# Optimization experiments

Hardware: AMD Instinct MI355X
Metric: run time of the kernel (lower is better)

## Reference

```python
import jax, jax.numpy as jnp
import numpy as np

B, L, D, H = 4, 1024, 1024, 16
HD = D // H
SCALE = 1.0 / np.sqrt(HD)
NOISE_PROB = 0.05
NOISE_SCALE = 0.1


def _linear(x, w, b):
    # torch nn.Linear convention: y = x @ W^T + b, W: [out, in]
    return x @ w.T + b


def _quantum_noise(key, real, imag, p=NOISE_PROB, s=NOISE_SCALE):
    """Phase flips, amplitude noise, and measurement dropout on a complex
    tensor represented as (real, imag). Deterministic given `key`."""
    k_phase, k_amp, k_nr, k_ni, k_meas = jax.random.split(key, 5)
    shape = real.shape
    flip = jnp.where(jax.random.uniform(k_phase, shape) < p, -1.0, 1.0)
    amp_mask = (jax.random.uniform(k_amp, shape) < p).astype(real.dtype)
    new_r = real * flip + jax.random.normal(k_nr, shape, real.dtype) * s * amp_mask
    new_i = imag * flip + jax.random.normal(k_ni, shape, imag.dtype) * s * amp_mask
    keep = 1.0 - (jax.random.uniform(k_meas, shape) < p * 0.5).astype(real.dtype)
    return new_r * keep, new_i * keep


def _heads(t):
    # [B, L, D] -> [B, H, L, HD]
    b, l, _ = t.shape
    return t.reshape(b, l, H, HD).transpose(0, 2, 1, 3)


def setup_inputs() -> dict:
    key = jax.random.key(0)
    ks = jax.random.split(key, 16)
    inp = {
        "x_real": jax.random.normal(ks[0], (B, L, D), jnp.float32),
        "x_imag": jax.random.normal(ks[1], (B, L, D), jnp.float32),
        "mask": jnp.ones((B, L), jnp.int32),
    }
    names = ["qr", "qi", "kr", "ki", "vr", "vi", "or", "oi"]
    for i, n in enumerate(names):
        inp[n + "_w"] = jax.random.normal(ks[2 + i], (D, D), jnp.float32) * 0.02
        inp[n + "_b"] = jnp.zeros((D,), jnp.float32)
    ent = jnp.eye(H) + (jax.random.normal(ks[10], (H, H)) * 0.1) * (
        jax.random.uniform(ks[11], (H, H)) < 0.2
    ).astype(jnp.float32)
    inp["ent"] = ent
    return inp


def reference(x_real, x_imag, mask, qr_w, qr_b, qi_w, qi_b, kr_w, kr_b,
              ki_w, ki_b, vr_w, vr_b, vi_w, vi_b, or_w, or_b, oi_w, oi_b, ent):
    # complex Q/K/V: real part from x.real, imag part from x.imag
    q_r, q_i = _linear(x_real, qr_w, qr_b), _linear(x_imag, qi_w, qi_b)
    k_r, k_i = _linear(x_real, kr_w, kr_b), _linear(x_imag, ki_w, ki_b)
    v_r, v_i = _linear(x_real, vr_w, vr_b), _linear(x_imag, vi_w, vi_b)

    nkey = jax.random.key(1)
    q_r, q_i = _quantum_noise(jax.random.fold_in(nkey, 0), q_r, q_i)
    k_r, k_i = _quantum_noise(jax.random.fold_in(nkey, 1), k_r, k_i)
    v_r, v_i = _quantum_noise(jax.random.fold_in(nkey, 2), v_r, v_i)

    q_r, q_i, k_r, k_i, v_r, v_i = map(_heads, (q_r, q_i, k_r, k_i, v_r, v_i))

    # torch.einsum('bhld,hh->bhld') == per-head scaling by diag(ent)
    d = jnp.diagonal(ent)[None, :, None, None]
    q_r, q_i = q_r * d, q_i * d
    k_r, k_i = k_r * d, k_i * d

    # Re(q . conj(k)) interference score: [B, H, Lq, Lk]
    scores = (jnp.einsum("bhqd,bhkd->bhqk", q_r, k_r)
              + jnp.einsum("bhqd,bhkd->bhqk", q_i, k_i)) * SCALE
    scores = jnp.where(mask[:, None, None, :] == 0, -1e9, scores)
    attn = jax.nn.softmax(scores, axis=-1)

    out_r = jnp.einsum("bhqk,bhkd->bhqd", attn, v_r)
    out_i = jnp.einsum("bhqk,bhkd->bhqd", attn, v_i)
    out_r = out_r.transpose(0, 2, 1, 3).reshape(x_real.shape)
    out_i = out_i.transpose(0, 2, 1, 3).reshape(x_real.shape)

    out_real = _linear(out_r, or_w, or_b)
    out_imag = _linear(out_i, oi_w, oi_b)
    return out_real, out_imag, attn
```

## Files before the change

### kernel.cpp

```cpp
#include <hip/hip_runtime.h>
#include <cstdint>

#define PARTITIONABLE 1

static constexpr int Bsz = 4, Lsz = 1024, Dsz = 1024, Hn = 16, HDsz = 64;
static constexpr size_t ELEMS = (size_t)Bsz * Lsz * Dsz;
static constexpr uint32_t HALF_N = (uint32_t)(ELEMS / 2);
static constexpr float SCALE = 0.125f;
static constexpr float P_NOISE = 0.05f;
static constexpr float S_NOISE = 0.1f;
static constexpr size_t MBy = 1024 * 1024;

typedef unsigned short u16;
typedef uint64_t u64;
typedef __attribute__((ext_vector_type(8))) short short8v;
typedef __attribute__((ext_vector_type(4))) float floatx4;
typedef __attribute__((ext_vector_type(4))) unsigned int uint4v;

__device__ __forceinline__ void gload16(const u16* g, u16* l) {
  __builtin_amdgcn_global_load_lds(
      (const __attribute__((address_space(1))) void*)(g),
      (__attribute__((address_space(3))) void*)(l), 16, 0, 0);
}

__host__ __device__ __forceinline__ void tf2x32(uint32_t k0, uint32_t k1,
                                                uint32_t x0, uint32_t x1,
                                                uint32_t& o0, uint32_t& o1) {
  uint32_t ks2 = k0 ^ k1 ^ 0x1BD11BDAu;
  x0 += k0; x1 += k1;
#define TFR(r) { x0 += x1; x1 = (x1 << (r)) | (x1 >> (32 - (r))); x1 ^= x0; }
  TFR(13) TFR(15) TFR(26) TFR(6)
  x0 += k1; x1 += ks2 + 1u;
  TFR(17) TFR(29) TFR(16) TFR(24)
  x0 += ks2; x1 += k0 + 2u;
  TFR(13) TFR(15) TFR(26) TFR(6)
  x0 += k0; x1 += k1 + 3u;
  TFR(17) TFR(29) TFR(16) TFR(24)
  x0 += k1; x1 += ks2 + 4u;
  TFR(13) TFR(15) TFR(26) TFR(6)
  x0 += ks2; x1 += k0 + 5u;
#undef TFR
  o0 = x0; o1 = x1;
}

struct KeySet { uint32_t k[5][2]; };
struct AllKeys { KeySet t[3]; };

__device__ __forceinline__ uint32_t draw_bits(uint32_t k0, uint32_t k1, uint32_t idx) {
#if PARTITIONABLE
  uint32_t o0, o1; tf2x32(k0, k1, 0u, idx, o0, o1);
  return o0 ^ o1;
#else
  uint32_t o0, o1;
  if (idx < HALF_N) { tf2x32(k0, k1, idx, idx + HALF_N, o0, o1); return o0; }
  tf2x32(k0, k1, idx - HALF_N, idx, o0, o1); return o1;
#endif
}

__device__ __forceinline__ float unif01(uint32_t bits) {
  return __uint_as_float((bits >> 9) | 0x3f800000u) - 1.0f;
}

__device__ __forceinline__ float normal_from_bits(uint32_t bits) {
  const float LO = -0.99999994f;
  float f = unif01(bits);
  float x = fmaxf(LO, f * 2.0f + LO);
  float w = -log1pf(-x * x);
  float p;
  if (w < 5.0f) {
    w = w - 2.5f;
    p = 2.81022636e-08f;
    p = fmaf(p, w, 3.43273939e-07f);
    p = fmaf(p, w, -3.5233877e-06f);
    p = fmaf(p, w, -4.39150654e-06f);
    p = fmaf(p, w, 0.00021858087f);
    p = fmaf(p, w, -0.00125372503f);
    p = fmaf(p, w, -0.00417768164f);
    p = fmaf(p, w, 0.246640727f);
    p = fmaf(p, w, 1.50140941f);
  } else {
    w = sqrtf(w) - 3.0f;
    p = -0.000200214257f;
    p = fmaf(p, w, 0.000100950558f);
    p = fmaf(p, w, 0.00134934322f);
    p = fmaf(p, w, -0.00367342844f);
    p = fmaf(p, w, 0.00573950773f);
    p = fmaf(p, w, -0.0076224613f);
    p = fmaf(p, w, 0.00943887047f);
    p = fmaf(p, w, 1.00167406f);
    p = fmaf(p, w, 2.83297682f);
  }
  return 1.41421356f * (p * x);
}

__device__ __forceinline__ uint32_t bf16_rn(float f) {
  uint32_t u = __float_as_uint(f);
  return (u + 0x7FFFu + ((u >> 16) & 1u)) >> 16;
}
__device__ __forceinline__ float bf2f(uint32_t h) { return __uint_as_float(h << 16); }
__device__ __forceinline__ void cvt_split(float4 v, u64& hi, u64& lo) {
  uint32_t h0 = bf16_rn(v.x), h1 = bf16_rn(v.y), h2 = bf16_rn(v.z), h3 = bf16_rn(v.w);
  float r0 = v.x - bf2f(h0), r1 = v.y - bf2f(h1), r2 = v.z - bf2f(h2), r3 = v.w - bf2f(h3);
  uint32_t l0 = bf16_rn(r0), l1 = bf16_rn(r1), l2 = bf16_rn(r2), l3 = bf16_rn(r3);
  hi = (u64)h0 | ((u64)h1 << 16) | ((u64)h2 << 32) | ((u64)h3 << 48);
  lo = (u64)l0 | ((u64)l1 << 16) | ((u64)l2 << 32) | ((u64)l3 << 48);
}

__device__ __forceinline__ void mfma_tile(const u16* Ahs, const u16* Als,
                                          const u16* Bhs, const u16* Bls,
                                          int l, int wm, int wn, floatx4 acc[4][4]) {
#pragma unroll
  for (int c = 0; c < 2; ++c) {
    const int pr = (l ^ (l >> 4) ^ (c << 2)) & 63;
    short8v aH[4], aL[4], bH[4], bL[4];
#pragma unroll
    for (int t = 0; t < 4; ++t) {
      const int ia = ((c * 8 + wm * 4 + t) * 64 + pr) * 8;
      aH[t] = *(const short8v*)&Ahs[ia]; aL[t] = *(const short8v*)&Als[ia];
      const int ib = ((c * 8 + wn * 4 + t) * 64 + pr) * 8;
      bH[t] = *(const short8v*)&Bhs[ib]; bL[t] = *(const short8v*)&Bls[ib];
    }
#pragma unroll
    for (int mt = 0; mt < 4; ++mt)
#pragma unroll
      for (int nt = 0; nt < 4; ++nt) {
        acc[mt][nt] = __builtin_amdgcn_mfma_f32_16x16x32_bf16(aH[mt], bH[nt], acc[mt][nt], 0, 0, 0);
        acc[mt][nt] = __builtin_amdgcn_mfma_f32_16x16x32_bf16(aH[mt], bL[nt], acc[mt][nt], 0, 0, 0);
        acc[mt][nt] = __builtin_amdgcn_mfma_f32_16x16x32_bf16(aL[mt], bH[nt], acc[mt][nt], 0, 0, 0);
      }
  }
}

__global__ __launch_bounds__(256) void split_kernel(const float* __restrict__ src,
                                                    u16* __restrict__ dh,
                                                    u16* __restrict__ dl, int n4) {
  int i = blockIdx.x * 256 + (int)threadIdx.x;
  if (i >= n4) return;
  float4 v = ((const float4*)src)[i];
  u64 h, l; cvt_split(v, h, l);
  ((u64*)dh)[i] = h; ((u64*)dl)[i] = l;
}

struct GJob { const u16* Ah; const u16* Al; const u16* Wh; const u16* Wl;
              const float* Wf; const float* bias; float* Yf; u16* Yh; u16* Yl; };
struct GJobs { GJob j[6]; };

template<int MODE>
__global__ __launch_bounds__(256, 2) void gemm_kernel(GJobs jobs) {
  const GJob J = jobs.j[blockIdx.z];
  const int n0 = blockIdx.x * 128, m0 = blockIdx.y * 128;
  __shared__ u16 Ahs[8192], Als[8192], Bhs[8192], Bls[8192];
  const int tid = (int)threadIdx.x;
  const int q_st = tid >> 4, kq = tid & 15;
  const int c_st = kq >> 3, m2s = (kq >> 1) & 3, half = kq & 1;
  const int p_st = (q_st + 16 * m2s) ^ m2s ^ (c_st << 2);
  const int stBase = c_st * 4096 + p_st * 8 + half * 4;
  const int w = tid >> 6, l = tid & 63;
  const int cA = w >> 1, m2A = l >> 4;
  const int qA = (l ^ m2A ^ (cA << 2)) & 15;
  const int colA = cA * 32 + m2A * 8;
  const int tb = (w & 1) * 4;
  const int wm = w >> 1, wn = w & 1;

  floatx4 acc[4][4];
#pragma unroll
  for (int i = 0; i < 4; ++i)
#pragma unroll
    for (int j = 0; j < 4; ++j) acc[i][j] = (floatx4){0.f, 0.f, 0.f, 0.f};

  const u16* ahp = J.Ah + (size_t)(m0 + qA) * Dsz + colA;
  const u16* alp = J.Al + (size_t)(m0 + qA) * Dsz + colA;
  const u16* whp = (MODE == 0) ? J.Wh + (size_t)(n0 + qA) * Dsz + colA : nullptr;
  const u16* wlp = (MODE == 0) ? J.Wl + (size_t)(n0 + qA) * Dsz + colA : nullptr;
  const float* wrow = (MODE == 1) ? J.Wf + (size_t)(n0 + q_st) * Dsz + kq * 4 : nullptr;

  for (int k0 = 0; k0 < Dsz; k0 += 64) {
    __syncthreads();
#pragma unroll
    for (int i = 0; i < 4; ++i) {
      const size_t go = (size_t)((tb + i) * 16) * Dsz + k0;
      gload16(ahp + go, &Ahs[(w * 4 + i) * 512]);
      gload16(alp + go, &Als[(w * 4 + i) * 512]);
      if (MODE == 0) {
        gload16(whp + go, &Bhs[(w * 4 + i) * 512]);
        gload16(wlp + go, &Bls[(w * 4 + i) * 512]);
      }
    }
    if (MODE == 1) {
#pragma unroll
      for (int rr = 0; rr < 8; ++rr) {
        float4 wb = *(const float4*)(wrow + (size_t)rr * 16 * Dsz + k0);
        u64 bh, bl; cvt_split(wb, bh, bl);
        const int off = stBase + rr * 512;
        *(u64*)&Bhs[off] = bh; *(u64*)&Bls[off] = bl;
      }
    }
    __syncthreads();
    mfma_tile(Ahs, Als, Bhs, Bls, l, wm, wn, acc);
  }
  const int colLane = l & 15, rquad = l >> 4;
#pragma unroll
  for (int nt = 0; nt < 4; ++nt) {
    const int col = n0 + wn * 64 + nt * 16 + colLane;
    const float bv = J.bias[col];
#pragma unroll
    for (int mt = 0; mt < 4; ++mt) {
      const int r0 = m0 + wm * 64 + mt * 16 + rquad * 4;
#pragma unroll
      for (int j = 0; j < 4; ++j) {
        float v = acc[mt][nt][j] + bv;
        if (MODE == 1) {
          J.Yf[(size_t)(r0 + j) * Dsz + col] = v;
        } else {
          uint32_t hi = bf16_rn(v);
          uint32_t lo = bf16_rn(v - bf2f(hi));
          J.Yh[(size_t)(r0 + j) * Dsz + col] = (u16)hi;
          J.Yl[(size_t)(r0 + j) * Dsz + col] = (u16)lo;
        }
      }
    }
  }
}

__global__ __launch_bounds__(256) void noise_kernel(
    u16* __restrict__ qhr, u16* __restrict__ qlr, u16* __restrict__ qhi, u16* __restrict__ qli,
    u16* __restrict__ khr, u16* __restrict__ klr, u16* __restrict__ khi, u16* __restrict__ kli,
    u16* __restrict__ vhr, u16* __restrict__ vlr, u16* __restrict__ vhi, u16* __restrict__ vli,
    const float* __restrict__ ent, AllKeys keys) {
  const uint32_t e = blockIdx.x * 256u + threadIdx.x;
  const int j = (int)blockIdx.y;
  u16 *rh, *rl, *ih, *il;
  if (j == 0) { rh = qhr; rl = qlr; ih = qhi; il = qli; }
  else if (j == 1) { rh = khr; rl = klr; ih = khi; il = kli; }
  else { rh = vhr; rl = vlr; ih = vhi; il = vli; }
  const KeySet& ks = keys.t[j];
  const uint32_t b_phase = draw_bits(ks.k[0][0], ks.k[0][1], e);
  const uint32_t b_amp   = draw_bits(ks.k[1][0], ks.k[1][1], e);
  const uint32_t b_nr    = draw_bits(ks.k[2][0], ks.k[2][1], e);
  const uint32_t b_ni    = draw_bits(ks.k[3][0], ks.k[3][1], e);
  const uint32_t b_meas  = draw_bits(ks.k[4][0], ks.k[4][1], e);
  const float flip = (unif01(b_phase) < P_NOISE) ? -1.0f : 1.0f;
  const float amp  = (unif01(b_amp)  < P_NOISE) ? 1.0f : 0.0f;
  const float keep = (unif01(b_meas) < P_NOISE * 0.5f) ? 0.0f : 1.0f;
  const float nr = normal_from_bits(b_nr);
  const float ni = normal_from_bits(b_ni);
  float r  = bf2f(rh[e]) + bf2f(rl[e]);
  float iv = bf2f(ih[e]) + bf2f(il[e]);
  r  = (r  * flip + nr * S_NOISE * amp) * keep;
  iv = (iv * flip + ni * S_NOISE * amp) * keep;
  if (j != 2) {
    const int h = ((int)e & (Dsz - 1)) >> 6;
    const float d = ent[h * Hn + h];
    r *= d; iv *= d;
  }
  uint32_t hr = bf16_rn(r);  rh[e] = (u16)hr; rl[e] = (u16)bf16_rn(r - bf2f(hr));
  uint32_t hi2 = bf16_rn(iv); ih[e] = (u16)hi2; il[e] = (u16)bf16_rn(iv - bf2f(hi2));
}

__global__ __launch_bounds__(256, 2) void scores_kernel(
    const u16* __restrict__ qhr, const u16* __restrict__ qlr,
    const u16* __restrict__ qhi, const u16* __restrict__ qli,
    const u16* __restrict__ khr, const u16* __restrict__ klr,
    const u16* __restrict__ khi, const u16* __restrict__ kli,
    const int* __restrict__ mask, float* __restrict__ attn) {
  const int bh = (int)blockIdx.z;
  const int b = bh >> 4, h = bh & 15;
  const int n0 = blockIdx.x * 128, m0 = blockIdx.y * 128;
  __shared__ u16 Ahs[8192], Als[8192], Bhs[8192], Bls[8192];
  const int tid = (int)threadIdx.x;
  const int w = tid >> 6, l = tid & 63;
  const int cA = w >> 1, m2A = l >> 4;
  const int qA = (l ^ m2A ^ (cA << 2)) & 15;
  const int colA = cA * 32 + m2A * 8;
  const int tb = (w & 1) * 4;
  const int wm = w >> 1, wn = w & 1;

  floatx4 acc[4][4];
#pragma unroll
  for (int i = 0; i < 4; ++i)
#pragma unroll
    for (int j = 0; j < 4; ++j) acc[i][j] = (floatx4){0.f, 0.f, 0.f, 0.f};

  const size_t abase = ((size_t)(b * Lsz) + m0 + qA) * Dsz + h * HDsz + colA;
  const size_t bbase = ((size_t)(b * Lsz) + n0 + qA) * Dsz + h * HDsz + colA;

#pragma unroll
  for (int s = 0; s < 2; ++s) {
    const u16* Ah = s ? qhi : qhr; const u16* Al = s ? qli : qlr;
    const u16* Bh = s ? khi : khr; const u16* Bl = s ? kli : klr;
    __syncthreads();
#pragma unroll
    for (int i = 0; i < 4; ++i) {
      const size_t go = (size_t)((tb + i) * 16) * Dsz;
      gload16(Ah + abase + go, &Ahs[(w * 4 + i) * 512]);
      gload16(Al + abase + go, &Als[(w * 4 + i) * 512]);
      gload16(Bh + bbase + go, &Bhs[(w * 4 + i) * 512]);
      gload16(Bl + bbase + go, &Bls[(w * 4 + i) * 512]);
    }
    __syncthreads();
    mfma_tile(Ahs, Als, Bhs, Bls, l, wm, wn, acc);
  }
  const int colLane = l & 15, rquad = l >> 4;
#pragma unroll
  for (int nt = 0; nt < 4; ++nt) {
    const int col = n0 + wn * 64 + nt * 16 + colLane;
    const int mv = mask[b * Lsz + col];
#pragma unroll
    for (int mt = 0; mt < 4; ++mt) {
      const int r0 = m0 + wm * 64 + mt * 16 + rquad * 4;
#pragma unroll
      for (int j = 0; j < 4; ++j)
        attn[((size_t)bh * Lsz + r0 + j) * Lsz + col] =
            (mv == 0) ? -1e9f : acc[mt][nt][j] * SCALE;
    }
  }
}

__global__ __launch_bounds__(256) void vtrans_kernel(
    const u16* __restrict__ vhr, const u16* __restrict__ vlr,
    const u16* __restrict__ vhi, const u16* __restrict__ vli,
    u16* __restrict__ vth, u16* __restrict__ vtl) {
  const int bh = (int)blockIdx.y;
  const int b = bh >> 4, h = bh & 15;
  const int k0 = blockIdx.x * 64;
  __shared__ uint32_t T[128 * 65];
  const int t = (int)threadIdx.x;
  const int krow = t >> 4, d4 = (t & 15) * 4;

#pragma unroll
  for (int src = 0; src < 2; ++src) {
    const u16* VH = src ? vhi : vhr;
    const u16* VL = src ? vli : vlr;
    const int nb = src * 64;
#pragma unroll
    for (int p = 0; p < 4; ++p) {
      const int k = p * 16 + krow;
      const size_t off = ((size_t)(b * Lsz) + k0 + k) * Dsz + h * HDsz + d4;
      u64 hv = *(const u64*)(VH + off);
      u64 lv = *(const u64*)(VL + off);
#pragma unroll
      for (int e = 0; e < 4; ++e) {
        uint32_t hi = (uint32_t)((hv >> (16 * e)) & 0xFFFFu);
        uint32_t lo = (uint32_t)((lv >> (16 * e)) & 0xFFFFu);
        T[(nb + d4 + e) * 65 + k] = lo | (hi << 16);
      }
    }
  }
  __syncthreads();
  const int n = t >> 1, hf = t & 1;
  const size_t rowb = ((size_t)bh * 128 + n) * Lsz + k0 + hf * 32;
#pragma unroll
  for (int g = 0; g < 4; ++g) {
    uint32_t wv[8];
#pragma unroll
    for (int u = 0; u < 8; ++u) wv[u] = T[n * 65 + hf * 32 + g * 8 + u];
    uint4v hvv, lvv;
    hvv.x = (wv[0] >> 16) | (wv[1] & 0xFFFF0000u);
    hvv.y = (wv[2] >> 16) | (wv[3] & 0xFFFF0000u);
    hvv.z = (wv[4] >> 16) | (wv[5] & 0xFFFF0000u);
    hvv.w = (wv[6] >> 16) | (wv[7] & 0xFFFF0000u);
    lvv.x = (wv[0] & 0xFFFFu) | (wv[1] << 16);
    lvv.y = (wv[2] & 0xFFFFu) | (wv[3] << 16);
    lvv.z = (wv[4] & 0xFFFFu) | (wv[5] << 16);
    lvv.w = (wv[6] & 0xFFFFu) | (wv[7] << 16);
    *(uint4v*)&vth[rowb + g * 8] = hvv;
    *(uint4v*)&vtl[rowb + g * 8] = lvv;
  }
}

__global__ __launch_bounds__(256) void rowstat_kernel(const float* __restrict__ S,
                                                      float* __restrict__ rowm,
                                                      float* __restrict__ rowsum) {
  const int wv = (int)threadIdx.x >> 6, lane = (int)threadIdx.x & 63;
  const size_t row = (size_t)blockIdx.x * 4 + wv;
  const float* p = S + row * Lsz;
  float4 v[4];
#pragma unroll
  for (int i = 0; i < 4; ++i) v[i] = *(const float4*)(p + i * 256 + lane * 4);
  float m = -3.402823466e38f;
#pragma unroll
  for (int i = 0; i < 4; ++i)
    m = fmaxf(m, fmaxf(fmaxf(v[i].x, v[i].y), fmaxf(v[i].z, v[i].w)));
#pragma unroll
  for (int d = 1; d < 64; d <<= 1) m = fmaxf(m, __shfl_xor(m, d));
  float s = 0.f;
#pragma unroll
  for (int i = 0; i < 4; ++i)
    s += expf(v[i].x - m) + expf(v[i].y - m) + expf(v[i].z - m) + expf(v[i].w - m);
#pragma unroll
  for (int d = 1; d < 64; d <<= 1) s += __shfl_xor(s, d);
  if (lane == 0) { rowm[row] = m; rowsum[row] = s; }
}

__global__ __launch_bounds__(256, 2) void pv_kernel(
    float* __restrict__ attn, const u16* __restrict__ vth, const u16* __restrict__ vtl,
    const float* __restrict__ rowm, const float* __restrict__ rowsum,
    u16* __restrict__ ohr, u16* __restrict__ olr,
    u16* __restrict__ ohi, u16* __restrict__ oli) {
  const int bh = (int)blockIdx.y;
  const int b = bh >> 4, h = bh & 15;
  const int m0 = blockIdx.x * 128;
  __shared__ u16 Ahs[8192], Als[8192], Bhs[8192], Bls[8192];
  const int tid = (int)threadIdx.x;
  const int q_st = tid >> 4, kq = tid & 15;
  const int c_st = kq >> 3, m2s = (kq >> 1) & 3, half = kq & 1;
  const int p_st = (q_st + 16 * m2s) ^ m2s ^ (c_st << 2);
  const int stBase = c_st * 4096 + p_st * 8 + half * 4;
  const int w = tid >> 6, l = tid & 63;
  const int cA = w >> 1, m2A = l >> 4;
  const int qA = (l ^ m2A ^ (cA << 2)) & 15;
  const int colA = cA * 32 + m2A * 8;
  const int tb = (w & 1) * 4;
  const int wm = w >> 1, wn = w & 1;

  float rmv[8], inv[8];
#pragma unroll
  for (int rr = 0; rr < 8; ++rr) {
    const int row = bh * Lsz + m0 + q_st + rr * 16;
    rmv[rr] = rowm[row]; inv[rr] = 1.0f / rowsum[row];
  }

  floatx4 acc[4][4];
#pragma unroll
  for (int i = 0; i < 4; ++i)
#pragma unroll
    for (int j = 0; j < 4; ++j) acc[i][j] = (floatx4){0.f, 0.f, 0.f, 0.f};

  float* arow = attn + ((size_t)bh * Lsz + m0 + q_st) * Lsz + kq * 4;
  const u16* bhp = vth + ((size_t)bh * 128 + qA) * Lsz + colA;
  const u16* blp = vtl + ((size_t)bh * 128 + qA) * Lsz + colA;

  for (int k0 = 0; k0 < Lsz; k0 += 64) {
    __syncthreads();
#pragma unroll
    for (int i = 0; i < 4; ++i) {
      const size_t go = (size_t)((tb + i) * 16) * Lsz + k0;
      gload16(bhp + go, &Bhs[(w * 4 + i) * 512]);
      gload16(blp + go, &Bls[(w * 4 + i) * 512]);
    }
#pragma unroll
    for (int rr = 0; rr < 8; ++rr) {
      float4 s4 = *(const float4*)(arow + (size_t)rr * 16 * Lsz + k0);
      float4 p4;
      p4.x = expf(s4.x - rmv[rr]) * inv[rr];
      p4.y = expf(s4.y - rmv[rr]) * inv[rr];
      p4.z = expf(s4.z - rmv[rr]) * inv[rr];
      p4.w = expf(s4.w - rmv[rr]) * inv[rr];
      *(float4*)(arow + (size_t)rr * 16 * Lsz + k0) = p4;
      u64 ah, al; cvt_split(p4, ah, al);
      const int off = stBase + rr * 512;
      *(u64*)&Ahs[off] = ah; *(u64*)&Als[off] = al;
    }
    __syncthreads();
    mfma_tile(Ahs, Als, Bhs, Bls, l, wm, wn, acc);
  }
  const int colLane = l & 15, rquad = l >> 4;
#pragma unroll
  for (int nt = 0; nt < 4; ++nt) {
    const int col = wn * 64 + nt * 16 + colLane;
    u16* oh = (col < 64) ? ohr : ohi;
    u16* ol = (col < 64) ? olr : oli;
    const int dcol = col & 63;
#pragma unroll
    for (int mt = 0; mt < 4; ++mt) {
      const int r0 = m0 + wm * 64 + mt * 16 + rquad * 4;
#pragma unroll
      for (int j = 0; j < 4; ++j) {
        float v = acc[mt][nt][j];
        uint32_t hi = bf16_rn(v);
        uint32_t lo = bf16_rn(v - bf2f(hi));
        const size_t oidx = ((size_t)(b * Lsz) + r0 + j) * Dsz + h * HDsz + dcol;
        oh[oidx] = (u16)hi; ol[oidx] = (u16)lo;
      }
    }
  }
}

extern "C" void kernel_launch(void* const* d_in, const int* in_sizes, int n_in,
                              void* d_out, int out_size, void* d_ws, size_t ws_size,
                              hipStream_t stream) {
  const float* x_real = (const float*)d_in[0];
  const float* x_imag = (const float*)d_in[1];
  const int*   mask   = (const int*)d_in[2];
  const float* pw[6] = {(const float*)d_in[3], (const float*)d_in[5], (const float*)d_in[7],
                        (const float*)d_in[9], (const float*)d_in[11], (const float*)d_in[13]};
  const float* pb[6] = {(const float*)d_in[4], (const float*)d_in[6], (const float*)d_in[8],
                        (const float*)d_in[10], (const float*)d_in[12], (const float*)d_in[14]};
  const float* or_w = (const float*)d_in[15]; const float* or_b = (const float*)d_in[16];
  const float* oi_w = (const float*)d_in[17]; const float* oi_b = (const float*)d_in[18];
  const float* ent  = (const float*)d_in[19];

  float* out_real = (float*)d_out;
  float* out_imag = out_real + ELEMS;
  float* attn     = out_imag + ELEMS;

  if (ws_size < 96 * MBy) return;
  uint8_t* wsb = (uint8_t*)d_ws;
  u16* qhr = (u16*)(wsb + 0 * MBy);  u16* qlr = (u16*)(wsb + 8 * MBy);
  u16* qhi = (u16*)(wsb + 16 * MBy); u16* qli = (u16*)(wsb + 24 * MBy);
  u16* khr = (u16*)(wsb + 32 * MBy); u16* klr = (u16*)(wsb + 40 * MBy);
  u16* khi = (u16*)(wsb + 48 * MBy); u16* kli = (u16*)(wsb + 56 * MBy);
  u16* xhr = (u16*)(wsb + 64 * MBy); u16* xlr = (u16*)(wsb + 72 * MBy);
  u16* xhi = (u16*)(wsb + 80 * MBy); u16* xli = (u16*)(wsb + 88 * MBy);
  u16* vth = (u16*)(wsb + 64 * MBy); u16* vtl = (u16*)(wsb + 80 * MBy);
  u16* ohr = (u16*)(wsb + 0 * MBy);  u16* olr = (u16*)(wsb + 8 * MBy);
  u16* ohi = (u16*)(wsb + 16 * MBy); u16* oli = (u16*)(wsb + 24 * MBy);

  uint8_t* atb = (uint8_t*)attn;
  u16* vhr = (u16*)(atb + 0 * MBy);  u16* vlr = (u16*)(atb + 8 * MBy);
  u16* vhi = (u16*)(atb + 16 * MBy); u16* vli = (u16*)(atb + 24 * MBy);

  float* rowm = out_real;
  float* rowsum = out_real + 65536;

  AllKeys keys;
  for (int j = 0; j < 3; ++j) {
    uint32_t a, b2;
    tf2x32(0u, 1u, 0u, (uint32_t)j, a, b2);
#if PARTITIONABLE
    for (int i = 0; i < 5; ++i)
      tf2x32(a, b2, 0u, (uint32_t)i, keys.t[j].k[i][0], keys.t[j].k[i][1]);
#else
    uint32_t out10[10];
    for (int i = 0; i < 5; ++i) {
      uint32_t o0, o1; tf2x32(a, b2, (uint32_t)i, (uint32_t)(i + 5), o0, o1);
      out10[i] = o0; out10[i + 5] = o1;
    }
    for (int i = 0; i < 5; ++i) { keys.t[j].k[i][0] = out10[2*i]; keys.t[j].k[i][1] = out10[2*i+1]; }
#endif
  }

  split_kernel<<<dim3(4096), 256, 0, stream>>>(x_real, xhr, xlr, (int)(ELEMS / 4));
  split_kernel<<<dim3(4096), 256, 0, stream>>>(x_imag, xhi, xli, (int)(ELEMS / 4));
  u16* pwh[6]; u16* pwl[6];
  for (int z = 0; z < 6; ++z) {
    pwh[z] = (u16*)(atb + 32 * MBy + (size_t)z * 4 * MBy);
    pwl[z] = pwh[z] + (size_t)Dsz * Dsz;
    split_kernel<<<dim3(1024), 256, 0, stream>>>(pw[z], pwh[z], pwl[z], Dsz * Dsz / 4);
  }

  GJobs pj{};
  u16* yh[6] = {qhr, qhi, khr, khi, vhr, vhi};
  u16* yl[6] = {qlr, qli, klr, kli, vlr, vli};
  const u16* ah6[6] = {xhr, xhi, xhr, xhi, xhr, xhi};
  const u16* al6[6] = {xlr, xli, xlr, xli, xlr, xli};
  for (int z = 0; z < 6; ++z) {
    pj.j[z].Ah = ah6[z]; pj.j[z].Al = al6[z];
    pj.j[z].Wh = pwh[z]; pj.j[z].Wl = pwl[z]; pj.j[z].Wf = nullptr;
    pj.j[z].bias = pb[z]; pj.j[z].Yf = nullptr; pj.j[z].Yh = yh[z]; pj.j[z].Yl = yl[z];
  }
  gemm_kernel<0><<<dim3(8, 32, 6), 256, 0, stream>>>(pj);

  noise_kernel<<<dim3((uint32_t)(ELEMS / 256), 3), 256, 0, stream>>>(
      qhr, qlr, qhi, qli, khr, klr, khi, kli, vhr, vlr, vhi, vli, ent, keys);

  vtrans_kernel<<<dim3(16, 64), 256, 0, stream>>>(vhr, vlr, vhi, vli, vth, vtl);

  scores_kernel<<<dim3(8, 8, 64), 256, 0, stream>>>(
      qhr, qlr, qhi, qli, khr, klr, khi, kli, mask, attn);

  rowstat_kernel<<<dim3(16384), 256, 0, stream>>>(attn, rowm, rowsum);

  pv_kernel<<<dim3(8, 64), 256, 0, stream>>>(attn, vth, vtl, rowm, rowsum,
                                             ohr, olr, ohi, oli);

  GJobs oj{};
  oj.j[0].Ah = ohr; oj.j[0].Al = olr; oj.j[0].Wf = or_w; oj.j[0].bias = or_b; oj.j[0].Yf = out_real;
  oj.j[1].Ah = ohi; oj.j[1].Al = oli; oj.j[1].Wf = oi_w; oj.j[1].bias = oi_b; oj.j[1].Yf = out_imag;
  gemm_kernel<1><<<dim3(8, 32, 2), 256, 0, stream>>>(oj);
}
```

Measured before the change: 796.8 us.

## Double-buffer GEMM tiles, fuse noise into projection epilogue, pre-split output weights

The GEMM, scores and PV kernels switch from single 64-wide K tiles to double-buffered 32-wide K tiles, so global-to-LDS loads for the next tile overlap the MFMAs on the current one. The separate noise kernel is removed: quantum noise and the per-head diagonal entanglement scale are applied in the QKV projection epilogue, which avoids a full read and rewrite of Q/K/V. The output projection now reads pre-split bf16 hi/lo weights from workspace instead of converting fp32 weights inside the GEMM loop. The costs are two extra split launches, more LDS-loop barriers, and the noise RNG work moving into the GEMM epilogue.

```diff
diff --git a/kernel.cpp b/kernel.cpp
--- a/kernel.cpp
+++ b/kernel.cpp
@@ -93,6 +93,18 @@
   return 1.41421356f * (p * x);
 }
 
+__device__ __forceinline__ float apply_noise(float v, const KeySet& ks, uint32_t e, int imag) {
+  const uint32_t b_phase = draw_bits(ks.k[0][0], ks.k[0][1], e);
+  const uint32_t b_amp   = draw_bits(ks.k[1][0], ks.k[1][1], e);
+  const uint32_t b_n     = draw_bits(ks.k[2 + imag][0], ks.k[2 + imag][1], e);
+  const uint32_t b_meas  = draw_bits(ks.k[4][0], ks.k[4][1], e);
+  const float flip = (unif01(b_phase) < P_NOISE) ? -1.0f : 1.0f;
+  const float amp  = (unif01(b_amp)  < P_NOISE) ? 1.0f : 0.0f;
+  const float keep = (unif01(b_meas) < P_NOISE * 0.5f) ? 0.0f : 1.0f;
+  const float n = normal_from_bits(b_n);
+  return (v * flip + n * S_NOISE * amp) * keep;
+}
+
 __device__ __forceinline__ uint32_t bf16_rn(float f) {
   uint32_t u = __float_as_uint(f);
   return (u + 0x7FFFu + ((u >> 16) & 1u)) >> 16;
@@ -106,29 +118,25 @@
   lo = (u64)l0 | ((u64)l1 << 16) | ((u64)l2 << 32) | ((u64)l3 << 48);
 }
 
-__device__ __forceinline__ void mfma_tile(const u16* Ahs, const u16* Als,
+__device__ __forceinline__ void mfma_step(const u16* Ahs, const u16* Als,
                                           const u16* Bhs, const u16* Bls,
-                                          int l, int wm, int wn, floatx4 acc[4][4]) {
-#pragma unroll
-  for (int c = 0; c < 2; ++c) {
-    const int pr = (l ^ (l >> 4) ^ (c << 2)) & 63;
-    short8v aH[4], aL[4], bH[4], bL[4];
-#pragma unroll
-    for (int t = 0; t < 4; ++t) {
-      const int ia = ((c * 8 + wm * 4 + t) * 64 + pr) * 8;
-      aH[t] = *(const short8v*)&Ahs[ia]; aL[t] = *(const short8v*)&Als[ia];
-      const int ib = ((c * 8 + wn * 4 + t) * 64 + pr) * 8;
-      bH[t] = *(const short8v*)&Bhs[ib]; bL[t] = *(const short8v*)&Bls[ib];
+                                          int pr, int wm, int wn, floatx4 acc[4][4]) {
+  short8v aH[4], aL[4], bH[4], bL[4];
+#pragma unroll
+  for (int t = 0; t < 4; ++t) {
+    const int ia = ((wm * 4 + t) * 64 + pr) * 8;
+    aH[t] = *(const short8v*)&Ahs[ia]; aL[t] = *(const short8v*)&Als[ia];
+    const int ib = ((wn * 4 + t) * 64 + pr) * 8;
+    bH[t] = *(const short8v*)&Bhs[ib]; bL[t] = *(const short8v*)&Bls[ib];
+  }
+#pragma unroll
+  for (int mt = 0; mt < 4; ++mt)
+#pragma unroll
+    for (int nt = 0; nt < 4; ++nt) {
+      acc[mt][nt] = __builtin_amdgcn_mfma_f32_16x16x32_bf16(aH[mt], bH[nt], acc[mt][nt], 0, 0, 0);
+      acc[mt][nt] = __builtin_amdgcn_mfma_f32_16x16x32_bf16(aH[mt], bL[nt], acc[mt][nt], 0, 0, 0);
+      acc[mt][nt] = __builtin_amdgcn_mfma_f32_16x16x32_bf16(aL[mt], bH[nt], acc[mt][nt], 0, 0, 0);
     }
-#pragma unroll
-    for (int mt = 0; mt < 4; ++mt)
-#pragma unroll
-      for (int nt = 0; nt < 4; ++nt) {
-        acc[mt][nt] = __builtin_amdgcn_mfma_f32_16x16x32_bf16(aH[mt], bH[nt], acc[mt][nt], 0, 0, 0);
-        acc[mt][nt] = __builtin_amdgcn_mfma_f32_16x16x32_bf16(aH[mt], bL[nt], acc[mt][nt], 0, 0, 0);
-        acc[mt][nt] = __builtin_amdgcn_mfma_f32_16x16x32_bf16(aL[mt], bH[nt], acc[mt][nt], 0, 0, 0);
-      }
-  }
 }
 
 __global__ __launch_bounds__(256) void split_kernel(const float* __restrict__ src,
@@ -142,119 +150,84 @@
 }
 
 struct GJob { const u16* Ah; const u16* Al; const u16* Wh; const u16* Wl;
-              const float* Wf; const float* bias; float* Yf; u16* Yh; u16* Yl; };
+              const float* bias; float* Yf; u16* Yh; u16* Yl;
+              int noise_sel;
+              int ent_scale; };
 struct GJobs { GJob j[6]; };
 
 template<int MODE>
-__global__ __launch_bounds__(256, 2) void gemm_kernel(GJobs jobs) {
+__global__ __launch_bounds__(256, 2) void gemm_kernel(GJobs jobs,
+                                                      const float* __restrict__ ent,
+                                                      AllKeys keys) {
   const GJob J = jobs.j[blockIdx.z];
   const int n0 = blockIdx.x * 128, m0 = blockIdx.y * 128;
-  __shared__ u16 Ahs[8192], Als[8192], Bhs[8192], Bls[8192];
-  const int tid = (int)threadIdx.x;
-  const int q_st = tid >> 4, kq = tid & 15;
-  const int c_st = kq >> 3, m2s = (kq >> 1) & 3, half = kq & 1;
-  const int p_st = (q_st + 16 * m2s) ^ m2s ^ (c_st << 2);
-  const int stBase = c_st * 4096 + p_st * 8 + half * 4;
-  const int w = tid >> 6, l = tid & 63;
-  const int cA = w >> 1, m2A = l >> 4;
-  const int qA = (l ^ m2A ^ (cA << 2)) & 15;
-  const int colA = cA * 32 + m2A * 8;
-  const int tb = (w & 1) * 4;
+  __shared__ u16 Ahs[2][4096], Als[2][4096], Bhs[2][4096], Bls[2][4096];
+  const int tid = (int)threadIdx.x, w = tid >> 6, l = tid & 63;
   const int wm = w >> 1, wn = w & 1;
-
-  floatx4 acc[4][4];
-#pragma unroll
-  for (int i = 0; i < 4; ++i)
-#pragma unroll
-    for (int j = 0; j < 4; ++j) acc[i][j] = (floatx4){0.f, 0.f, 0.f, 0.f};
+  const int qA = (l ^ (l >> 4)) & 15, colA = (l >> 4) * 8;
+  const int pr = (l ^ (l >> 4)) & 63;
+  const int t0 = w * 2, t1 = w * 2 + 1;
 
   const u16* ahp = J.Ah + (size_t)(m0 + qA) * Dsz + colA;
   const u16* alp = J.Al + (size_t)(m0 + qA) * Dsz + colA;
-  const u16* whp = (MODE == 0) ? J.Wh + (size_t)(n0 + qA) * Dsz + colA : nullptr;
-  const u16* wlp = (MODE == 0) ? J.Wl + (size_t)(n0 + qA) * Dsz + colA : nullptr;
-  const float* wrow = (MODE == 1) ? J.Wf + (size_t)(n0 + q_st) * Dsz + kq * 4 : nullptr;
-
-  for (int k0 = 0; k0 < Dsz; k0 += 64) {
+  const u16* whp = J.Wh + (size_t)(n0 + qA) * Dsz + colA;
+  const u16* wlp = J.Wl + (size_t)(n0 + qA) * Dsz + colA;
+
+  floatx4 acc[4][4];
+#pragma unroll
+  for (int i = 0; i < 4; ++i)
+#pragma unroll
+    for (int j = 0; j < 4; ++j) acc[i][j] = (floatx4){0.f, 0.f, 0.f, 0.f};
+
+#define STG(bufi, K0V) { \
+    const size_t g0 = (size_t)(t0 * 16) * Dsz + (K0V); \
+    const size_t g1 = (size_t)(t1 * 16) * Dsz + (K0V); \
+    gload16(ahp + g0, &Ahs[bufi][t0 * 512]); gload16(ahp + g1, &Ahs[bufi][t1 * 512]); \
+    gload16(alp + g0, &Als[bufi][t0 * 512]); gload16(alp + g1, &Als[bufi][t1 * 512]); \
+    gload16(whp + g0, &Bhs[bufi][t0 * 512]); gload16(whp + g1, &Bhs[bufi][t1 * 512]); \
+    gload16(wlp + g0, &Bls[bufi][t0 * 512]); gload16(wlp + g1, &Bls[bufi][t1 * 512]); }
+
+  STG(0, 0)
+  __syncthreads();
+  for (int kt = 0; kt < 32; kt += 2) {
+    if (kt + 1 < 32) STG(1, (size_t)(kt + 1) * 32)
+    mfma_step(Ahs[0], Als[0], Bhs[0], Bls[0], pr, wm, wn, acc);
     __syncthreads();
-#pragma unroll
-    for (int i = 0; i < 4; ++i) {
-      const size_t go = (size_t)((tb + i) * 16) * Dsz + k0;
-      gload16(ahp + go, &Ahs[(w * 4 + i) * 512]);
-      gload16(alp + go, &Als[(w * 4 + i) * 512]);
-      if (MODE == 0) {
-        gload16(whp + go, &Bhs[(w * 4 + i) * 512]);
-        gload16(wlp + go, &Bls[(w * 4 + i) * 512]);
-      }
-    }
-    if (MODE == 1) {
-#pragma unroll
-      for (int rr = 0; rr < 8; ++rr) {
-        float4 wb = *(const float4*)(wrow + (size_t)rr * 16 * Dsz + k0);
-        u64 bh, bl; cvt_split(wb, bh, bl);
-        const int off = stBase + rr * 512;
-        *(u64*)&Bhs[off] = bh; *(u64*)&Bls[off] = bl;
-      }
-    }
+    if (kt + 2 < 32) STG(0, (size_t)(kt + 2) * 32)
+    mfma_step(Ahs[1], Als[1], Bhs[1], Bls[1], pr, wm, wn, acc);
     __syncthreads();
-    mfma_tile(Ahs, Als, Bhs, Bls, l, wm, wn, acc);
-  }
+  }
+#undef STG
+
   const int colLane = l & 15, rquad = l >> 4;
 #pragma unroll
   for (int nt = 0; nt < 4; ++nt) {
     const int col = n0 + wn * 64 + nt * 16 + colLane;
     const float bv = J.bias[col];
+    float dscale = 1.0f;
+    if (MODE == 0 && J.ent_scale) { const int hh = col >> 6; dscale = ent[hh * Hn + hh]; }
 #pragma unroll
     for (int mt = 0; mt < 4; ++mt) {
       const int r0 = m0 + wm * 64 + mt * 16 + rquad * 4;
 #pragma unroll
-      for (int j = 0; j < 4; ++j) {
-        float v = acc[mt][nt][j] + bv;
+      for (int j2 = 0; j2 < 4; ++j2) {
+        float v = acc[mt][nt][j2] + bv;
         if (MODE == 1) {
-          J.Yf[(size_t)(r0 + j) * Dsz + col] = v;
+          J.Yf[(size_t)(r0 + j2) * Dsz + col] = v;
         } else {
-          uint32_t hi = bf16_rn(v);
-          uint32_t lo = bf16_rn(v - bf2f(hi));
-          J.Yh[(size_t)(r0 + j) * Dsz + col] = (u16)hi;
-          J.Yl[(size_t)(r0 + j) * Dsz + col] = (u16)lo;
+          if (J.noise_sel >= 0) {
+            const uint32_t e = (uint32_t)(r0 + j2) * 1024u + (uint32_t)col;
+            v = apply_noise(v, keys.t[J.noise_sel >> 1], e, J.noise_sel & 1);
+            v *= dscale;
+          }
+          const uint32_t hi = bf16_rn(v);
+          const uint32_t lo = bf16_rn(v - bf2f(hi));
+          J.Yh[(size_t)(r0 + j2) * Dsz + col] = (u16)hi;
+          J.Yl[(size_t)(r0 + j2) * Dsz + col] = (u16)lo;
         }
       }
     }
   }
-}
-
-__global__ __launch_bounds__(256) void noise_kernel(
-    u16* __restrict__ qhr, u16* __restrict__ qlr, u16* __restrict__ qhi, u16* __restrict__ qli,
-    u16* __restrict__ khr, u16* __restrict__ klr, u16* __restrict__ khi, u16* __restrict__ kli,
-    u16* __restrict__ vhr, u16* __restrict__ vlr, u16* __restrict__ vhi, u16* __restrict__ vli,
-    const float* __restrict__ ent, AllKeys keys) {
-  const uint32_t e = blockIdx.x * 256u + threadIdx.x;
-  const int j = (int)blockIdx.y;
-  u16 *rh, *rl, *ih, *il;
-  if (j == 0) { rh = qhr; rl = qlr; ih = qhi; il = qli; }
-  else if (j == 1) { rh = khr; rl = klr; ih = khi; il = kli; }
-  else { rh = vhr; rl = vlr; ih = vhi; il = vli; }
-  const KeySet& ks = keys.t[j];
-  const uint32_t b_phase = draw_bits(ks.k[0][0], ks.k[0][1], e);
-  const uint32_t b_amp   = draw_bits(ks.k[1][0], ks.k[1][1], e);
-  const uint32_t b_nr    = draw_bits(ks.k[2][0], ks.k[2][1], e);
-  const uint32_t b_ni    = draw_bits(ks.k[3][0], ks.k[3][1], e);
-  const uint32_t b_meas  = draw_bits(ks.k[4][0], ks.k[4][1], e);
-  const float flip = (unif01(b_phase) < P_NOISE) ? -1.0f : 1.0f;
-  const float amp  = (unif01(b_amp)  < P_NOISE) ? 1.0f : 0.0f;
-  const float keep = (unif01(b_meas) < P_NOISE * 0.5f) ? 0.0f : 1.0f;
-  const float nr = normal_from_bits(b_nr);
-  const float ni = normal_from_bits(b_ni);
-  float r  = bf2f(rh[e]) + bf2f(rl[e]);
-  float iv = bf2f(ih[e]) + bf2f(il[e]);
-  r  = (r  * flip + nr * S_NOISE * amp) * keep;
-  iv = (iv * flip + ni * S_NOISE * amp) * keep;
-  if (j != 2) {
-    const int h = ((int)e & (Dsz - 1)) >> 6;
-    const float d = ent[h * Hn + h];
-    r *= d; iv *= d;
-  }
-  uint32_t hr = bf16_rn(r);  rh[e] = (u16)hr; rl[e] = (u16)bf16_rn(r - bf2f(hr));
-  uint32_t hi2 = bf16_rn(iv); ih[e] = (u16)hi2; il[e] = (u16)bf16_rn(iv - bf2f(hi2));
 }
 
 __global__ __launch_bounds__(256, 2) void scores_kernel(
@@ -266,14 +239,15 @@
   const int bh = (int)blockIdx.z;
   const int b = bh >> 4, h = bh & 15;
   const int n0 = blockIdx.x * 128, m0 = blockIdx.y * 128;
-  __shared__ u16 Ahs[8192], Als[8192], Bhs[8192], Bls[8192];
-  const int tid = (int)threadIdx.x;
-  const int w = tid >> 6, l = tid & 63;
-  const int cA = w >> 1, m2A = l >> 4;
-  const int qA = (l ^ m2A ^ (cA << 2)) & 15;
-  const int colA = cA * 32 + m2A * 8;
-  const int tb = (w & 1) * 4;
+  __shared__ u16 Ahs[2][4096], Als[2][4096], Bhs[2][4096], Bls[2][4096];
+  const int tid = (int)threadIdx.x, w = tid >> 6, l = tid & 63;
   const int wm = w >> 1, wn = w & 1;
+  const int qA = (l ^ (l >> 4)) & 15, colA = (l >> 4) * 8;
+  const int pr = (l ^ (l >> 4)) & 63;
+  const int t0 = w * 2, t1 = w * 2 + 1;
+
+  const size_t aoff = ((size_t)(b * Lsz) + m0 + qA) * Dsz + h * HDsz + colA;
+  const size_t boff = ((size_t)(b * Lsz) + n0 + qA) * Dsz + h * HDsz + colA;
 
   floatx4 acc[4][4];
 #pragma unroll
@@ -281,25 +255,28 @@
 #pragma unroll
     for (int j = 0; j < 4; ++j) acc[i][j] = (floatx4){0.f, 0.f, 0.f, 0.f};
 
-  const size_t abase = ((size_t)(b * Lsz) + m0 + qA) * Dsz + h * HDsz + colA;
-  const size_t bbase = ((size_t)(b * Lsz) + n0 + qA) * Dsz + h * HDsz + colA;
-
-#pragma unroll
-  for (int s = 0; s < 2; ++s) {
-    const u16* Ah = s ? qhi : qhr; const u16* Al = s ? qli : qlr;
-    const u16* Bh = s ? khi : khr; const u16* Bl = s ? kli : klr;
-    __syncthreads();
-#pragma unroll
-    for (int i = 0; i < 4; ++i) {
-      const size_t go = (size_t)((tb + i) * 16) * Dsz;
-      gload16(Ah + abase + go, &Ahs[(w * 4 + i) * 512]);
-      gload16(Al + abase + go, &Als[(w * 4 + i) * 512]);
-      gload16(Bh + bbase + go, &Bhs[(w * 4 + i) * 512]);
-      gload16(Bl + bbase + go, &Bls[(w * 4 + i) * 512]);
-    }
-    __syncthreads();
-    mfma_tile(Ahs, Als, Bhs, Bls, l, wm, wn, acc);
-  }
+#define STGS(bufi, AH, AL, BH, BL, K0V) { \
+    const size_t g0 = (size_t)(t0 * 16) * Dsz + (K0V); \
+    const size_t g1 = (size_t)(t1 * 16) * Dsz + (K0V); \
+    gload16(AH + aoff + g0, &Ahs[bufi][t0 * 512]); gload16(AH + aoff + g1, &Ahs[bufi][t1 * 512]); \
+    gload16(AL + aoff + g0, &Als[bufi][t0 * 512]); gload16(AL + aoff + g1, &Als[bufi][t1 * 512]); \
+    gload16(BH + boff + g0, &Bhs[bufi][t0 * 512]); gload16(BH + boff + g1, &Bhs[bufi][t1 * 512]); \
+    gload16(BL + boff + g0, &Bls[bufi][t0 * 512]); gload16(BL + boff + g1, &Bls[bufi][t1 * 512]); }
+
+  STGS(0, qhr, qlr, khr, klr, 0)
+  __syncthreads();
+  STGS(1, qhr, qlr, khr, klr, 32)
+  mfma_step(Ahs[0], Als[0], Bhs[0], Bls[0], pr, wm, wn, acc);
+  __syncthreads();
+  STGS(0, qhi, qli, khi, kli, 0)
+  mfma_step(Ahs[1], Als[1], Bhs[1], Bls[1], pr, wm, wn, acc);
+  __syncthreads();
+  STGS(1, qhi, qli, khi, kli, 32)
+  mfma_step(Ahs[0], Als[0], Bhs[0], Bls[0], pr, wm, wn, acc);
+  __syncthreads();
+  mfma_step(Ahs[1], Als[1], Bhs[1], Bls[1], pr, wm, wn, acc);
+#undef STGS
+
   const int colLane = l & 15, rquad = l >> 4;
 #pragma unroll
   for (int nt = 0; nt < 4; ++nt) {
@@ -400,60 +377,78 @@
   const int bh = (int)blockIdx.y;
   const int b = bh >> 4, h = bh & 15;
   const int m0 = blockIdx.x * 128;
-  __shared__ u16 Ahs[8192], Als[8192], Bhs[8192], Bls[8192];
-  const int tid = (int)threadIdx.x;
-  const int q_st = tid >> 4, kq = tid & 15;
-  const int c_st = kq >> 3, m2s = (kq >> 1) & 3, half = kq & 1;
-  const int p_st = (q_st + 16 * m2s) ^ m2s ^ (c_st << 2);
-  const int stBase = c_st * 4096 + p_st * 8 + half * 4;
-  const int w = tid >> 6, l = tid & 63;
-  const int cA = w >> 1, m2A = l >> 4;
-  const int qA = (l ^ m2A ^ (cA << 2)) & 15;
-  const int colA = cA * 32 + m2A * 8;
-  const int tb = (w & 1) * 4;
+  __shared__ u16 Ahs[2][4096], Als[2][4096], Bhs[2][4096], Bls[2][4096];
+  const int tid = (int)threadIdx.x, w = tid >> 6, l = tid & 63;
   const int wm = w >> 1, wn = w & 1;
-
-  float rmv[8], inv[8];
-#pragma unroll
-  for (int rr = 0; rr < 8; ++rr) {
-    const int row = bh * Lsz + m0 + q_st + rr * 16;
-    rmv[rr] = rowm[row]; inv[rr] = 1.0f / rowsum[row];
-  }
-
-  floatx4 acc[4][4];
-#pragma unroll
-  for (int i = 0; i < 4; ++i)
-#pragma unroll
-    for (int j = 0; j < 4; ++j) acc[i][j] = (floatx4){0.f, 0.f, 0.f, 0.f};
-
-  float* arow = attn + ((size_t)bh * Lsz + m0 + q_st) * Lsz + kq * 4;
+  const int qA = (l ^ (l >> 4)) & 15, colA = (l >> 4) * 8;
+  const int pr = (l ^ (l >> 4)) & 63;
+  const int t0 = w * 2, t1 = w * 2 + 1;
+
+  const int ar = tid >> 3, akq = tid & 7;
+  const int am2 = akq >> 1, ahalf = akq & 1;
+  int aidx[4];
+  float rmv[4], inv[4];
+#pragma unroll
+  for (int rr = 0; rr < 4; ++rr) {
+    const int trow = ar + rr * 32;
+    const int p = ((trow & 15) + 16 * am2) ^ am2;
+    aidx[rr] = ((trow >> 4) * 64 + p) * 8 + ahalf * 4;
+    const size_t grow = (size_t)bh * Lsz + m0 + trow;
+    rmv[rr] = rowm[grow]; inv[rr] = 1.0f / rowsum[grow];
+  }
+  float* arp = attn + ((size_t)bh * Lsz + m0 + ar) * Lsz + akq * 4;
   const u16* bhp = vth + ((size_t)bh * 128 + qA) * Lsz + colA;
   const u16* blp = vtl + ((size_t)bh * 128 + qA) * Lsz + colA;
 
-  for (int k0 = 0; k0 < Lsz; k0 += 64) {
+  floatx4 acc[4][4];
+#pragma unroll
+  for (int i = 0; i < 4; ++i)
+#pragma unroll
+    for (int j = 0; j < 4; ++j) acc[i][j] = (floatx4){0.f, 0.f, 0.f, 0.f};
+
+#define STGB(bufi, K0V) { \
+    const size_t g0 = (size_t)(t0 * 16) * Lsz + (K0V); \
+    const size_t g1 = (size_t)(t1 * 16) * Lsz + (K0V); \
+    gload16(bhp + g0, &Bhs[bufi][t0 * 512]); gload16(bhp + g1, &Bhs[bufi][t1 * 512]); \
+    gload16(blp + g0, &Bls[bufi][t0 * 512]); gload16(blp + g1, &Bls[bufi][t1 * 512]); }
+
+#define LOADA(K0V, A4) { \
+    _Pragma("unroll") for (int rr = 0; rr < 4; ++rr) \
+      A4[rr] = *(const float4*)(arp + (size_t)(rr * 32) * Lsz + (K0V)); }
+
+#define PROCA(bufi, K0V, A4) { \
+    _Pragma("unroll") for (int rr = 0; rr < 4; ++rr) { \
+      float4 p4; \
+      p4.x = expf(A4[rr].x - rmv[rr]) * inv[rr]; \
+      p4.y = expf(A4[rr].y - rmv[rr]) * inv[rr]; \
+      p4.z = expf(A4[rr].z - rmv[rr]) * inv[rr]; \
+      p4.w = expf(A4[rr].w - rmv[rr]) * inv[rr]; \
+      *(float4*)(arp + (size_t)(rr * 32) * Lsz + (K0V)) = p4; \
+      u64 h64, l64; cvt_split(p4, h64, l64); \
+      *(u64*)&Ahs[bufi][aidx[rr]] = h64; *(u64*)&Als[bufi][aidx[rr]] = l64; } }
+
+  {
+    float4 a4[4];
+    LOADA(0, a4)
+    STGB(0, 0)
+    PROCA(0, 0, a4)
+  }
+  __syncthreads();
+  for (int kt = 0; kt < 32; kt += 2) {
+    float4 n4[4];
+    if (kt + 1 < 32) { LOADA((size_t)(kt + 1) * 32, n4) STGB(1, (size_t)(kt + 1) * 32) }
+    mfma_step(Ahs[0], Als[0], Bhs[0], Bls[0], pr, wm, wn, acc);
+    if (kt + 1 < 32) PROCA(1, (size_t)(kt + 1) * 32, n4)
     __syncthreads();
-#pragma unroll
-    for (int i = 0; i < 4; ++i) {
-      const size_t go = (size_t)((tb + i) * 16) * Lsz + k0;
-      gload16(bhp + go, &Bhs[(w * 4 + i) * 512]);
-      gload16(blp + go, &Bls[(w * 4 + i) * 512]);
-    }
-#pragma unroll
-    for (int rr = 0; rr < 8; ++rr) {
-      float4 s4 = *(const float4*)(arow + (size_t)rr * 16 * Lsz + k0);
-      float4 p4;
-      p4.x = expf(s4.x - rmv[rr]) * inv[rr];
-      p4.y = expf(s4.y - rmv[rr]) * inv[rr];
-      p4.z = expf(s4.z - rmv[rr]) * inv[rr];
-      p4.w = expf(s4.w - rmv[rr]) * inv[rr];
-      *(float4*)(arow + (size_t)rr * 16 * Lsz + k0) = p4;
-      u64 ah, al; cvt_split(p4, ah, al);
-      const int off = stBase + rr * 512;
-      *(u64*)&Ahs[off] = ah; *(u64*)&Als[off] = al;
-    }
+    if (kt + 2 < 32) { LOADA((size_t)(kt + 2) * 32, n4) STGB(0, (size_t)(kt + 2) * 32) }
+    mfma_step(Ahs[1], Als[1], Bhs[1], Bls[1], pr, wm, wn, acc);
+    if (kt + 2 < 32) PROCA(0, (size_t)(kt + 2) * 32, n4)
     __syncthreads();
-    mfma_tile(Ahs, Als, Bhs, Bls, l, wm, wn, acc);
-  }
+  }
+#undef STGB
+#undef LOADA
+#undef PROCA
+
   const int colLane = l & 15, rquad = l >> 4;
 #pragma unroll
   for (int nt = 0; nt < 4; ++nt) {
@@ -467,8 +462,8 @@
 #pragma unroll
       for (int j = 0; j < 4; ++j) {
         float v = acc[mt][nt][j];
-        uint32_t hi = bf16_rn(v);
-        uint32_t lo = bf16_rn(v - bf2f(hi));
+        const uint32_t hi = bf16_rn(v);
+        const uint32_t lo = bf16_rn(v - bf2f(hi));
         const size_t oidx = ((size_t)(b * Lsz) + r0 + j) * Dsz + h * HDsz + dcol;
         oh[oidx] = (u16)hi; ol[oidx] = (u16)lo;
       }
@@ -505,6 +500,8 @@
   u16* vth = (u16*)(wsb + 64 * MBy); u16* vtl = (u16*)(wsb + 80 * MBy);
   u16* ohr = (u16*)(wsb + 0 * MBy);  u16* olr = (u16*)(wsb + 8 * MBy);
   u16* ohi = (u16*)(wsb + 16 * MBy); u16* oli = (u16*)(wsb + 24 * MBy);
+  u16* owh[2] = {(u16*)(wsb + 32 * MBy), (u16*)(wsb + 36 * MBy)};
+  u16* owl[2] = {(u16*)(wsb + 34 * MBy), (u16*)(wsb + 38 * MBy)};
 
   uint8_t* atb = (uint8_t*)attn;
   u16* vhr = (u16*)(atb + 0 * MBy);  u16* vlr = (u16*)(atb + 8 * MBy);
@@ -544,28 +541,33 @@
   u16* yl[6] = {qlr, qli, klr, kli, vlr, vli};
   const u16* ah6[6] = {xhr, xhi, xhr, xhi, xhr, xhi};
   const u16* al6[6] = {xlr, xli, xlr, xli, xlr, xli};
+  const int nsel[6] = {0, 1, 2, 3, 4, 5};
+  const int escl[6] = {1, 1, 1, 1, 0, 0};
   for (int z = 0; z < 6; ++z) {
     pj.j[z].Ah = ah6[z]; pj.j[z].Al = al6[z];
-    pj.j[z].Wh = pwh[z]; pj.j[z].Wl = pwl[z]; pj.j[z].Wf = nullptr;
+    pj.j[z].Wh = pwh[z]; pj.j[z].Wl = pwl[z];
     pj.j[z].bias = pb[z]; pj.j[z].Yf = nullptr; pj.j[z].Yh = yh[z]; pj.j[z].Yl = yl[z];
-  }
-  gemm_kernel<0><<<dim3(8, 32, 6), 256, 0, stream>>>(pj);
-
-  noise_kernel<<<dim3((uint32_t)(ELEMS / 256), 3), 256, 0, stream>>>(
-      qhr, qlr, qhi, qli, khr, klr, khi, kli, vhr, vlr, vhi, vli, ent, keys);
+    pj.j[z].noise_sel = nsel[z]; pj.j[z].ent_scale = escl[z];
+  }
+  gemm_kernel<0><<<dim3(8, 32, 6), 256, 0, stream>>>(pj, ent, keys);
 
   vtrans_kernel<<<dim3(16, 64), 256, 0, stream>>>(vhr, vlr, vhi, vli, vth, vtl);
 
   scores_kernel<<<dim3(8, 8, 64), 256, 0, stream>>>(
       qhr, qlr, qhi, qli, khr, klr, khi, kli, mask, attn);
 
+  split_kernel<<<dim3(1024), 256, 0, stream>>>(or_w, owh[0], owl[0], Dsz * Dsz / 4);
+  split_kernel<<<dim3(1024), 256, 0, stream>>>(oi_w, owh[1], owl[1], Dsz * Dsz / 4);
+
   rowstat_kernel<<<dim3(16384), 256, 0, stream>>>(attn, rowm, rowsum);
 
   pv_kernel<<<dim3(8, 64), 256, 0, stream>>>(attn, vth, vtl, rowm, rowsum,
                                              ohr, olr, ohi, oli);
 
   GJobs oj{};
-  oj.j[0].Ah = ohr; oj.j[0].Al = olr; oj.j[0].Wf = or_w; oj.j[0].bias = or_b; oj.j[0].Yf = out_real;
-  oj.j[1].Ah = ohi; oj.j[1].Al = oli; oj.j[1].Wf = oi_w; oj.j[1].bias = oi_b; oj.j[1].Yf = out_imag;
-  gemm_kernel<1><<<dim3(8, 32, 2), 256, 0, stream>>>(oj);
-}
+  oj.j[0].Ah = ohr; oj.j[0].Al = olr; oj.j[0].Wh = owh[0]; oj.j[0].Wl = owl[0];
+  oj.j[0].bias = or_b; oj.j[0].Yf = out_real; oj.j[0].noise_sel = -1; oj.j[0].ent_scale = 0;
+  oj.j[1].Ah = ohi; oj.j[1].Al = oli; oj.j[1].Wh = owh[1]; oj.j[1].Wl = owl[1];
+  oj.j[1].bias = oi_b; oj.j[1].Yf = out_imag; oj.j[1].noise_sel = -1; oj.j[1].ent_scale = 0;
+  gemm_kernel<1><<<dim3(8, 32, 2), 256, 0, stream>>>(oj, ent, keys);
+}
```

Result: slower. 955.3 us (+19.9%).
